# Kernel tuning notes

Measured on AMD Instinct MI355X. Metric: run time of the kernel, lower is better.

Reference implementation:

```python
import jax, jax.numpy as jnp
import numpy as np

E, NH, G = 2048, 16, 4
HD = E // NH          # head_dim = 128
KV = E // G           # kv proj width = 512 == G * HD
B, S = 2, 2048


def setup_inputs() -> dict:
    key = jax.random.key(0)
    ks = jax.random.split(key, 7)
    s = lambda n: 1.0 / np.sqrt(n)
    return {
        "query": jax.random.normal(ks[0], (B, S, E), jnp.float32),
        "key_in": jax.random.normal(ks[1], (B, S, E), jnp.float32),
        "value": jax.random.normal(ks[2], (B, S, E), jnp.float32),
        "Wq": jax.random.normal(ks[3], (E, E), jnp.float32) * s(E),
        "bq": jnp.zeros((E,), jnp.float32),
        "Wk": jax.random.normal(ks[4], (E, KV), jnp.float32) * s(E),
        "bk": jnp.zeros((KV,), jnp.float32),
        "Wv": jax.random.normal(ks[5], (E, KV), jnp.float32) * s(E),
        "bv": jnp.zeros((KV,), jnp.float32),
        "Wo": jax.random.normal(ks[6], (E, E), jnp.float32) * s(E),
        "bo": jnp.zeros((E,), jnp.float32),
    }


def reference(query, key_in, value, Wq, bq, Wk, bk, Wv, bv, Wo, bo):
    b, s, _ = query.shape
    scale = HD ** -0.5
    # projections
    q = (query @ Wq + bq).reshape(b, s, NH, HD).transpose(0, 2, 1, 3)   # [B,NH,S,HD]
    k = (key_in @ Wk + bk).reshape(b, s, G, HD).transpose(0, 2, 1, 3)   # [B,G,S,HD]
    v = (value @ Wv + bv).reshape(b, s, G, HD).transpose(0, 2, 1, 3)    # [B,G,S,HD]
    # grouped-query attention: each KV head serves NH//G query heads
    qg = q.reshape(b, G, NH // G, s, HD)                                # [B,G,NH/G,S,HD]
    scores = jnp.einsum('bgqsh,bgth->bgqst', qg, k) * scale             # [B,G,NH/G,S,S]
    w = jax.nn.softmax(scores, axis=-1)
    out = jnp.einsum('bgqst,bgth->bgqsh', w, v)                         # [B,G,NH/G,S,HD]
    out = out.reshape(b, NH, s, HD).transpose(0, 2, 1, 3).reshape(b, s, E)
    return out @ Wo + bo
```

## Files before the change

kernel.cpp:

```cpp
#include <hip/hip_runtime.h>
#include <hip/hip_bf16.h>

#define E_ 2048
#define S_ 2048
#define B_ 2
#define BS_ 4096
#define KV_ 512
#define NH_ 16
#define G_ 4
#define HD_ 128
#define QK_SCALE 0.08838834764831845f
#define LOG2E_ 1.4426950408889634f

typedef __attribute__((ext_vector_type(8))) short short8;
typedef __attribute__((ext_vector_type(4))) float floatx4;
typedef __attribute__((ext_vector_type(4))) unsigned short ushort4_;

static __device__ __forceinline__ unsigned short f2bf(float f) {
  unsigned int u = __builtin_bit_cast(unsigned int, f);
  u += 0x7fffu + ((u >> 16) & 1u);
  return (unsigned short)(u >> 16);
}

static __device__ __forceinline__ unsigned int cvt_pk_bf16(float lo, float hi) {
  unsigned int r;
  asm("v_cvt_pk_bf16_f32 %0, %1, %2" : "=v"(r) : "v"(lo), "v"(hi));
  return r;
}

static __device__ __forceinline__ void gld16(const void* g, void* l) {
  __builtin_amdgcn_global_load_lds(
      (const __attribute__((address_space(1))) unsigned int*)g,
      (__attribute__((address_space(3))) unsigned int*)l, 16, 0, 0);
}

__global__ __launch_bounds__(256) void k_prep(
    const float* __restrict__ Wq, unsigned short* __restrict__ WqT,
    const float* __restrict__ Wk, unsigned short* __restrict__ WkT,
    const float* __restrict__ Wv, unsigned short* __restrict__ WvT,
    const float* __restrict__ Wo, unsigned short* __restrict__ WoT) {
  __shared__ float ts[32][33];
  int t = blockIdx.x;
  const float* in; unsigned short* out; int N; int rem;
  if (t < 4096)      { in = Wq; out = WqT; N = 2048; rem = t; }
  else if (t < 5120) { in = Wk; out = WkT; N = 512;  rem = t - 4096; }
  else if (t < 6144) { in = Wv; out = WvT; N = 512;  rem = t - 5120; }
  else               { in = Wo; out = WoT; N = 2048; rem = t - 6144; }
  const int K = 2048;
  int nx = N >> 5;
  int bx = rem % nx, by = rem / nx;
  int tx = threadIdx.x & 31, ty = threadIdx.x >> 5;
  int n0 = bx * 32, k0 = by * 32;
#pragma unroll
  for (int i = 0; i < 4; ++i)
    ts[ty + i * 8][tx] = in[(size_t)(k0 + ty + i * 8) * N + n0 + tx];
  __syncthreads();
#pragma unroll
  for (int i = 0; i < 4; ++i)
    out[(size_t)(n0 + ty + i * 8) * K + k0 + tx] = f2bf(ts[tx][ty + i * 8]);
}

template <bool OUT_F32, bool A_F32, bool B_F32>
static __device__ __forceinline__ void gemm_bt_tile(
    const void* __restrict__ A, const void* __restrict__ Bt,
    const float* __restrict__ bias, bool rowBias, void* __restrict__ C,
    int N, int K, float scale, int bx, int by,
    unsigned short* As, unsigned short* Bs) {
  const int tid = threadIdx.x;
  const int w = tid >> 6;
  const int lhi = (tid >> 4) & 3;
  const int llo = tid & 15;
  const int wr = w >> 1, wc = w & 1;
  const size_t brow = (size_t)by * 128, bcol = (size_t)bx * 128;
  constexpr int ASTR = A_F32 ? 8192 : 4096;
  constexpr int BSTR = B_F32 ? 8192 : 4096;

  auto stage = [&](int k0, int bufi) {
    if constexpr (A_F32) {
#pragma unroll
      for (int i = 0; i < 4; ++i) {
        int o = i * 256 + tid;
        int row = o >> 3, gs = (o & 7) ^ (row & 7);
        gld16((const float*)A + (brow + row) * (size_t)K + k0 + gs * 4,
              As + bufi * ASTR + (size_t)(i * 256 + w * 64) * 8);
      }
    } else {
#pragma unroll
      for (int i = 0; i < 2; ++i) {
        int o = i * 256 + tid;
        int row = o >> 2, gs = (o & 3) ^ ((row >> 1) & 3);
        gld16((const unsigned short*)A + (brow + row) * (size_t)K + k0 + gs * 8,
              As + bufi * ASTR + (size_t)(i * 256 + w * 64) * 8);
      }
    }
    if constexpr (B_F32) {
#pragma unroll
      for (int i = 0; i < 4; ++i) {
        int o = i * 256 + tid;
        int row = o >> 3, gs = (o & 7) ^ (row & 7);
        gld16((const float*)Bt + (bcol + row) * (size_t)K + k0 + gs * 4,
              Bs + bufi * BSTR + (size_t)(i * 256 + w * 64) * 8);
      }
    } else {
#pragma unroll
      for (int i = 0; i < 2; ++i) {
        int o = i * 256 + tid;
        int row = o >> 2, gs = (o & 3) ^ ((row >> 1) & 3);
        gld16((const unsigned short*)Bt + (bcol + row) * (size_t)K + k0 + gs * 8,
              Bs + bufi * BSTR + (size_t)(i * 256 + w * 64) * 8);
      }
    }
  };

  auto frag_f32 = [&](const unsigned short* buf, int row) -> short8 {
    const char* p = (const char*)buf;
    int g0 = (lhi * 2) ^ (row & 7);
    float4 v0 = *reinterpret_cast<const float4*>(p + row * 128 + g0 * 16);
    float4 v1 = *reinterpret_cast<const float4*>(p + row * 128 + (g0 ^ 1) * 16);
    uint4 pk = {cvt_pk_bf16(v0.x, v0.y), cvt_pk_bf16(v0.z, v0.w),
                cvt_pk_bf16(v1.x, v1.y), cvt_pk_bf16(v1.z, v1.w)};
    return __builtin_bit_cast(short8, pk);
  };
  auto frag_bf = [&](const unsigned short* buf, int row) -> short8 {
    int g = lhi ^ ((row >> 1) & 3);
    return *reinterpret_cast<const short8*>((const char*)buf + row * 64 + g * 16);
  };

  floatx4 acc[4][4];
#pragma unroll
  for (int i = 0; i < 4; ++i)
#pragma unroll
    for (int j = 0; j < 4; ++j)
      acc[i][j] = (floatx4){0.f, 0.f, 0.f, 0.f};

  stage(0, 0);
  __syncthreads();
  int buf = 0;
  const int nk = K >> 5;
  for (int t = 0; t < nk; ++t) {
    if (t + 1 < nk) stage((t + 1) * 32, buf ^ 1);
    const unsigned short* Ab = As + buf * ASTR;
    const unsigned short* Bb = Bs + buf * BSTR;
    short8 a[4], b[4];
#pragma unroll
    for (int f = 0; f < 4; ++f) {
      int ra = wr * 64 + f * 16 + llo;
      int rb = wc * 64 + f * 16 + llo;
      if constexpr (A_F32)
        a[f] = frag_f32(Ab, ra);
      else
        a[f] = frag_bf(Ab, ra);
      if constexpr (B_F32)
        b[f] = frag_f32(Bb, rb);
      else
        b[f] = frag_bf(Bb, rb);
    }
    __builtin_amdgcn_s_setprio(1);
#pragma unroll
    for (int i = 0; i < 4; ++i)
#pragma unroll
      for (int j = 0; j < 4; ++j)
        acc[i][j] = __builtin_amdgcn_mfma_f32_16x16x32_bf16(a[i], b[j], acc[i][j], 0, 0, 0);
    __builtin_amdgcn_s_setprio(0);
    __syncthreads();
    buf ^= 1;
  }

  float* reg = reinterpret_cast<float*>(As) + w * 2048;
#pragma unroll
  for (int h = 0; h < 2; ++h) {
#pragma unroll
    for (int i2 = 0; i2 < 2; ++i2) {
      int i = h * 2 + i2;
#pragma unroll
      for (int j = 0; j < 4; ++j) {
#pragma unroll
        for (int r = 0; r < 4; ++r) {
          int row32 = i2 * 16 + lhi * 4 + r;
          int colx = (j * 16 + llo) ^ (lhi * 16);
          size_t grow = brow + wr * 64 + h * 32 + row32;
          size_t gc = bcol + wc * 64 + j * 16 + llo;
          float v = acc[i][j][r];
          v += rowBias ? bias[grow] : bias[gc];
          v *= scale;
          reg[row32 * 64 + colx] = v;
        }
      }
    }
#pragma unroll
    for (int p = 0; p < 8; ++p) {
      int r4 = (tid & 63) >> 4;
      int ch = tid & 15;
      int row32 = p * 4 + r4;
      int colx = (ch * 4) ^ ((p & 3) * 16);
      float4 v4 = *reinterpret_cast<const float4*>(reg + row32 * 64 + colx);
      size_t grow = brow + wr * 64 + h * 32 + row32;
      size_t gc = bcol + wc * 64 + ch * 4;
      if constexpr (OUT_F32) {
        *reinterpret_cast<float4*>((float*)C + grow * N + gc) = v4;
      } else {
        uint2 pk2;
        pk2.x = cvt_pk_bf16(v4.x, v4.y);
        pk2.y = cvt_pk_bf16(v4.z, v4.w);
        *reinterpret_cast<uint2*>((unsigned short*)C + grow * N + gc) = pk2;
      }
    }
  }
}

__global__ __launch_bounds__(256) void k_gemm_qkv(
    const float* __restrict__ query, const unsigned short* __restrict__ WqT,
    const float* __restrict__ bq, unsigned short* __restrict__ qb,
    const float* __restrict__ key_in, const unsigned short* __restrict__ WkT,
    const float* __restrict__ bk, unsigned short* __restrict__ kb,
    const unsigned short* __restrict__ WvT, const float* __restrict__ value,
    const float* __restrict__ bv, unsigned short* __restrict__ vtb) {
  __shared__ __align__(16) unsigned short lds[24576];
  int bid = blockIdx.x;
  if (bid < 512) {
    int xcd = bid & 7, u = bid >> 3;
    int by = (xcd >> 1) * 8 + (u & 7);
    int bx = (xcd & 1) * 8 + (u >> 3);
    gemm_bt_tile<false, true, false>(query, WqT, bq, false, qb, E_, E_,
                                     QK_SCALE * LOG2E_, bx, by,
                                     lds, lds + 16384);
  } else if (bid < 640) {
    int u = bid - 512;
    int cm = (u & 7) * 16 + (u >> 3);
    gemm_bt_tile<false, true, false>(key_in, WkT, bk, false, kb, KV_, E_, 1.0f,
                                     cm >> 5, cm & 31, lds, lds + 16384);
  } else {
    int u = bid - 640;
    int cm = (u & 7) * 16 + (u >> 3);
    gemm_bt_tile<false, false, true>(WvT, value, bv, true, vtb, BS_, E_, 1.0f,
                                     cm >> 2, cm & 3, lds, lds + 8192);
  }
}

__global__ __launch_bounds__(256) void k_gemm_o(
    const unsigned short* __restrict__ A, const unsigned short* __restrict__ Bt,
    const float* __restrict__ bias, float* __restrict__ C) {
  __shared__ __align__(16) unsigned short lds[16384];
  int cm = (blockIdx.x & 7) * 64 + (blockIdx.x >> 3);
  gemm_bt_tile<true, false, false>(A, Bt, bias, false, C, E_, E_, 1.0f,
                                   cm >> 5, cm & 31, lds, lds + 8192);
}

__global__ __launch_bounds__(512) void k_attn(
    const unsigned short* __restrict__ qb, const unsigned short* __restrict__ kb,
    const unsigned short* __restrict__ vt, unsigned short* __restrict__ attn) {
  __shared__ __align__(16) unsigned short Ks[2][64 * 128];
  __shared__ __align__(16) unsigned short Vs[2][128 * 64];
  __shared__ __align__(16) unsigned short Ps[8][32 * 64];

  const int tid = threadIdx.x;
  const int w = tid >> 6;
  const int lhi = (tid >> 4) & 3;
  const int llo = tid & 15;
  const int bid = blockIdx.x;
  const int xcd = bid & 7;
  const int b = xcd >> 2, g = xcd & 3;
  const int inner = bid >> 3;
  const int hq = inner & 3, qt = inner >> 2;
  const int h = g * 4 + hq;

  char* PsW = (char*)&Ps[0][0] + w * 4096;

  short8 qf[2][4];
#pragma unroll
  for (int rt = 0; rt < 2; ++rt)
#pragma unroll
    for (int hc = 0; hc < 4; ++hc) {
      int row = qt * 256 + w * 32 + rt * 16 + llo;
      qf[rt][hc] = *reinterpret_cast<const short8*>(
          qb + ((size_t)(b * 2048 + row)) * 2048 + h * 128 + hc * 32 + lhi * 8);
    }

  floatx4 acc[2][8];
#pragma unroll
  for (int rt = 0; rt < 2; ++rt)
#pragma unroll
    for (int dc = 0; dc < 8; ++dc)
      acc[rt][dc] = (floatx4){0.f, 0.f, 0.f, 0.f};
  float m_[2] = {-1e30f, -1e30f};
  float l_[2] = {0.f, 0.f};

  auto stage = [&](int kv0, int buf) {
#pragma unroll
    for (int i = 0; i < 2; ++i) {
      int o = i * 512 + tid;
      int row = o >> 4, gr2 = (o & 15) ^ (row & 7);
      gld16(kb + ((size_t)(b * 2048 + kv0 + row)) * 512 + g * 128 + gr2 * 8,
            &Ks[buf][(size_t)(i * 512 + w * 64) * 8]);
    }
#pragma unroll
    for (int i = 0; i < 2; ++i) {
      int o = i * 512 + tid;
      int row = o >> 3, gr2 = (o & 7) ^ (row & 7);
      gld16(vt + ((size_t)(g * 128 + row)) * 4096 + b * 2048 + kv0 + gr2 * 8,
            &Vs[buf][(size_t)(i * 512 + w * 64) * 8]);
    }
  };

  stage(0, 0);
  __syncthreads();
  int buf = 0;

  for (int t = 0; t < 32; ++t) {
    const int kv0 = t * 64;
    if (t < 31) stage(kv0 + 64, buf ^ 1);

    floatx4 sc[2][4];
#pragma unroll
    for (int rt = 0; rt < 2; ++rt)
#pragma unroll
      for (int c = 0; c < 4; ++c)
        sc[rt][c] = (floatx4){0.f, 0.f, 0.f, 0.f};
    __builtin_amdgcn_s_setprio(1);
#pragma unroll
    for (int c = 0; c < 4; ++c) {
      int krow = c * 16 + llo;
#pragma unroll
      for (int hc = 0; hc < 4; ++hc) {
        int byteoff = krow * 256 + ((hc * 64 + lhi * 16) ^ ((krow & 7) << 4));
        short8 kf = *reinterpret_cast<const short8*>((const char*)&Ks[buf][0] + byteoff);
        sc[0][c] = __builtin_amdgcn_mfma_f32_16x16x32_bf16(kf, qf[0][hc], sc[0][c], 0, 0, 0);
        sc[1][c] = __builtin_amdgcn_mfma_f32_16x16x32_bf16(kf, qf[1][hc], sc[1][c], 0, 0, 0);
      }
    }
    __builtin_amdgcn_s_setprio(0);

#pragma unroll
    for (int rt = 0; rt < 2; ++rt) {
      float pm = sc[rt][0][0];
#pragma unroll
      for (int c = 0; c < 4; ++c)
#pragma unroll
        for (int r = 0; r < 4; ++r) pm = fmaxf(pm, sc[rt][c][r]);
      if (__any(pm > m_[rt] + 8.0f)) {
        float t2 = pm;
        t2 = fmaxf(t2, __shfl_xor(t2, 16));
        t2 = fmaxf(t2, __shfl_xor(t2, 32));
        float m2 = fmaxf(m_[rt], t2);
        float scr = __builtin_amdgcn_exp2f(m_[rt] - m2);
        m_[rt] = m2;
        l_[rt] *= scr;
#pragma unroll
        for (int r = 0; r < 4; ++r) {
          float s_r = __shfl(scr, (tid & 48) | (((tid >> 2) & 12) + r));
#pragma unroll
          for (int dc = 0; dc < 8; ++dc) acc[rt][dc][r] *= s_r;
        }
      }
      float lsum = l_[rt];
#pragma unroll
      for (int c = 0; c < 4; ++c) {
        float e0 = __builtin_amdgcn_exp2f(sc[rt][c][0] - m_[rt]);
        float e1 = __builtin_amdgcn_exp2f(sc[rt][c][1] - m_[rt]);
        float e2 = __builtin_amdgcn_exp2f(sc[rt][c][2] - m_[rt]);
        float e3 = __builtin_amdgcn_exp2f(sc[rt][c][3] - m_[rt]);
        lsum += (e0 + e1) + (e2 + e3);
        uint2 pk;
        pk.x = cvt_pk_bf16(e0, e1);
        pk.y = cvt_pk_bf16(e2, e3);
        int byteoff = (rt * 16 + llo) * 128 + ((c * 32 + lhi * 8) ^ ((llo & 7) << 4));
        *reinterpret_cast<uint2*>(PsW + byteoff) = pk;
      }
      l_[rt] = lsum;
    }

    short8 pf[2][2];
#pragma unroll
    for (int rt = 0; rt < 2; ++rt)
#pragma unroll
      for (int kc = 0; kc < 2; ++kc) {
        int byteoff = (rt * 16 + llo) * 128 + ((kc * 64 + lhi * 16) ^ ((llo & 7) << 4));
        pf[rt][kc] = *reinterpret_cast<const short8*>(PsW + byteoff);
      }
    __builtin_amdgcn_s_setprio(1);
#pragma unroll
    for (int dc = 0; dc < 8; ++dc) {
      int vrow = dc * 16 + llo;
      int bo0 = vrow * 128 + ((lhi * 16) ^ ((vrow & 7) << 4));
      int bo1 = vrow * 128 + ((64 + lhi * 16) ^ ((vrow & 7) << 4));
      short8 vf0 = *reinterpret_cast<const short8*>((const char*)&Vs[buf][0] + bo0);
      short8 vf1 = *reinterpret_cast<const short8*>((const char*)&Vs[buf][0] + bo1);
      acc[0][dc] = __builtin_amdgcn_mfma_f32_16x16x32_bf16(pf[0][0], vf0, acc[0][dc], 0, 0, 0);
      acc[1][dc] = __builtin_amdgcn_mfma_f32_16x16x32_bf16(pf[1][0], vf0, acc[1][dc], 0, 0, 0);
      acc[0][dc] = __builtin_amdgcn_mfma_f32_16x16x32_bf16(pf[0][1], vf1, acc[0][dc], 0, 0, 0);
      acc[1][dc] = __builtin_amdgcn_mfma_f32_16x16x32_bf16(pf[1][1], vf1, acc[1][dc], 0, 0, 0);
    }
    __builtin_amdgcn_s_setprio(0);
    __syncthreads();
    buf ^= 1;
  }

#pragma unroll
  for (int rt = 0; rt < 2; ++rt) {
    float t2 = l_[rt];
    t2 += __shfl_xor(t2, 16);
    t2 += __shfl_xor(t2, 32);
    float linv = 1.0f / t2;
    float lr[4];
#pragma unroll
    for (int r = 0; r < 4; ++r)
      lr[r] = __shfl(linv, (tid & 48) | (((tid >> 2) & 12) + r));
    unsigned short* pw = (unsigned short*)PsW;
#pragma unroll
    for (int dc = 0; dc < 8; ++dc) {
      int pg = dc ^ lhi;
#pragma unroll
      for (int r = 0; r < 4; ++r)
        pw[(lhi * 4 + r) * 128 + pg * 16 + llo] = f2bf(acc[rt][dc][r] * lr[r]);
    }
    int lane = tid & 63;
#pragma unroll
    for (int p = 0; p < 4; ++p) {
      int row = p * 4 + (lane >> 4);
      int ch = lane & 15;
      uint4 v = *reinterpret_cast<const uint4*>(PsW + row * 256 + ch * 16);
      int dc = (ch >> 1) ^ (row >> 2);
      int grow = qt * 256 + w * 32 + rt * 16 + row;
      *reinterpret_cast<uint4*>(attn + ((size_t)(b * 2048 + grow)) * 2048 +
                                h * 128 + dc * 16 + (ch & 1) * 8) = v;
    }
  }
}

extern "C" void kernel_launch(void* const* d_in, const int* in_sizes, int n_in,
                              void* d_out, int out_size, void* d_ws, size_t ws_size,
                              hipStream_t stream) {
  const float* query  = (const float*)d_in[0];
  const float* key_in = (const float*)d_in[1];
  const float* value  = (const float*)d_in[2];
  const float* Wq = (const float*)d_in[3];
  const float* bq = (const float*)d_in[4];
  const float* Wk = (const float*)d_in[5];
  const float* bk = (const float*)d_in[6];
  const float* Wv = (const float*)d_in[7];
  const float* bv = (const float*)d_in[8];
  const float* Wo = (const float*)d_in[9];
  const float* bo = (const float*)d_in[10];
  float* out = (float*)d_out;

  char* ws = (char*)d_ws;
  size_t off = 0;
  auto alloc = [&](size_t bytes) {
    char* p = ws + off;
    off += (bytes + 255) & ~(size_t)255;
    return p;
  };
  unsigned short* WqT  = (unsigned short*)alloc((size_t)E_ * E_ * 2);
  unsigned short* WkT  = (unsigned short*)alloc((size_t)KV_ * E_ * 2);
  unsigned short* WvT  = (unsigned short*)alloc((size_t)KV_ * E_ * 2);
  unsigned short* WoT  = (unsigned short*)alloc((size_t)E_ * E_ * 2);
  unsigned short* qb   = (unsigned short*)alloc((size_t)BS_ * E_ * 2);
  unsigned short* kb   = (unsigned short*)alloc((size_t)BS_ * KV_ * 2);
  unsigned short* vtb  = (unsigned short*)alloc((size_t)KV_ * BS_ * 2);
  unsigned short* attb = (unsigned short*)alloc((size_t)BS_ * E_ * 2);

  k_prep<<<10240, 256, 0, stream>>>(Wq, WqT, Wk, WkT, Wv, WvT, Wo, WoT);
  k_gemm_qkv<<<768, 256, 0, stream>>>(query, WqT, bq, qb, key_in, WkT, bk, kb,
                                      WvT, value, bv, vtb);
  k_attn<<<B_ * NH_ * (S_ / 256), 512, 0, stream>>>(qb, kb, vtb, attb);
  k_gemm_o<<<512, 256, 0, stream>>>(attb, WoT, bo, out);
}
```

Baseline: 215.5 us.

## Load bf16 weight fragments directly from global memory, staging only one operand in LDS

The GEMM tile helper now stages only one operand through LDS: the fp32 activation for the QKV modes, or the bf16 A operand for the output projection. The other bf16 operand is read per-wave straight from global memory into MFMA fragments. This shrinks LDS use in the QKV kernel (from 24576 to 16384 shorts), which may allow more blocks per CU, and cuts LDS traffic. In exchange, the direct loads are uncoalesced 16-byte reads that happen every k-step without prefetch and rely on L2/L1 hits, and each wave pair reloads the same weight rows.

After: 294.8 us. 36.8% more time.

```diff
diff --git a/kernel.cpp b/kernel.cpp
--- a/kernel.cpp
+++ b/kernel.cpp
@@ -60,54 +60,40 @@
     out[(size_t)(n0 + ty + i * 8) * K + k0 + tx] = f2bf(ts[tx][ty + i * 8]);
 }
 
-template <bool OUT_F32, bool A_F32, bool B_F32>
-static __device__ __forceinline__ void gemm_bt_tile(
+template <int MODE>
+static __device__ __forceinline__ void gemm_tile(
     const void* __restrict__ A, const void* __restrict__ Bt,
     const float* __restrict__ bias, bool rowBias, void* __restrict__ C,
-    int N, int K, float scale, int bx, int by,
-    unsigned short* As, unsigned short* Bs) {
+    int N, int K, float scale, int bx, int by, unsigned short* lds) {
   const int tid = threadIdx.x;
   const int w = tid >> 6;
   const int lhi = (tid >> 4) & 3;
   const int llo = tid & 15;
   const int wr = w >> 1, wc = w & 1;
   const size_t brow = (size_t)by * 128, bcol = (size_t)bx * 128;
-  constexpr int ASTR = A_F32 ? 8192 : 4096;
-  constexpr int BSTR = B_F32 ? 8192 : 4096;
+
+  const float* fsrc = (MODE == 0) ? (const float*)A : (const float*)Bt;
+  const size_t fbase = (MODE == 0) ? brow : bcol;
+  const unsigned short* dsrc =
+      (MODE == 1) ? (const unsigned short*)A : (const unsigned short*)Bt;
+  const size_t dbase = (MODE == 1) ? (brow + wr * 64) : (bcol + wc * 64);
 
   auto stage = [&](int k0, int bufi) {
-    if constexpr (A_F32) {
-#pragma unroll
-      for (int i = 0; i < 4; ++i) {
-        int o = i * 256 + tid;
-        int row = o >> 3, gs = (o & 7) ^ (row & 7);
-        gld16((const float*)A + (brow + row) * (size_t)K + k0 + gs * 4,
-              As + bufi * ASTR + (size_t)(i * 256 + w * 64) * 8);
-      }
-    } else {
+    if constexpr (MODE == 2) {
 #pragma unroll
       for (int i = 0; i < 2; ++i) {
         int o = i * 256 + tid;
         int row = o >> 2, gs = (o & 3) ^ ((row >> 1) & 3);
         gld16((const unsigned short*)A + (brow + row) * (size_t)K + k0 + gs * 8,
-              As + bufi * ASTR + (size_t)(i * 256 + w * 64) * 8);
-      }
-    }
-    if constexpr (B_F32) {
+              lds + bufi * 4096 + (size_t)(i * 256 + w * 64) * 8);
+      }
+    } else {
 #pragma unroll
       for (int i = 0; i < 4; ++i) {
         int o = i * 256 + tid;
         int row = o >> 3, gs = (o & 7) ^ (row & 7);
-        gld16((const float*)Bt + (bcol + row) * (size_t)K + k0 + gs * 4,
-              Bs + bufi * BSTR + (size_t)(i * 256 + w * 64) * 8);
-      }
-    } else {
-#pragma unroll
-      for (int i = 0; i < 2; ++i) {
-        int o = i * 256 + tid;
-        int row = o >> 2, gs = (o & 3) ^ ((row >> 1) & 3);
-        gld16((const unsigned short*)Bt + (bcol + row) * (size_t)K + k0 + gs * 8,
-              Bs + bufi * BSTR + (size_t)(i * 256 + w * 64) * 8);
+        gld16(fsrc + (fbase + row) * (size_t)K + k0 + gs * 4,
+              lds + bufi * 8192 + (size_t)(i * 256 + w * 64) * 8);
       }
     }
   };
@@ -125,6 +111,10 @@
     int g = lhi ^ ((row >> 1) & 3);
     return *reinterpret_cast<const short8*>((const char*)buf + row * 64 + g * 16);
   };
+  auto dfrag = [&](int k0, int f) -> short8 {
+    return *reinterpret_cast<const short8*>(
+        dsrc + (dbase + f * 16 + llo) * (size_t)K + k0 + lhi * 8);
+  };
 
   floatx4 acc[4][4];
 #pragma unroll
@@ -138,35 +128,38 @@
   int buf = 0;
   const int nk = K >> 5;
   for (int t = 0; t < nk; ++t) {
-    if (t + 1 < nk) stage((t + 1) * 32, buf ^ 1);
-    const unsigned short* Ab = As + buf * ASTR;
-    const unsigned short* Bb = Bs + buf * BSTR;
-    short8 a[4], b[4];
+    const int k0 = t * 32;
+    if (t + 1 < nk) stage(k0 + 32, buf ^ 1);
+    short8 d[4];
+#pragma unroll
+    for (int f = 0; f < 4; ++f) d[f] = dfrag(k0, f);
+    short8 s[4];
 #pragma unroll
     for (int f = 0; f < 4; ++f) {
-      int ra = wr * 64 + f * 16 + llo;
-      int rb = wc * 64 + f * 16 + llo;
-      if constexpr (A_F32)
-        a[f] = frag_f32(Ab, ra);
+      if constexpr (MODE == 0)
+        s[f] = frag_f32(lds + buf * 8192, wr * 64 + f * 16 + llo);
+      else if constexpr (MODE == 1)
+        s[f] = frag_f32(lds + buf * 8192, wc * 64 + f * 16 + llo);
       else
-        a[f] = frag_bf(Ab, ra);
-      if constexpr (B_F32)
-        b[f] = frag_f32(Bb, rb);
-      else
-        b[f] = frag_bf(Bb, rb);
+        s[f] = frag_bf(lds + buf * 4096, wr * 64 + f * 16 + llo);
     }
     __builtin_amdgcn_s_setprio(1);
 #pragma unroll
     for (int i = 0; i < 4; ++i)
 #pragma unroll
-      for (int j = 0; j < 4; ++j)
-        acc[i][j] = __builtin_amdgcn_mfma_f32_16x16x32_bf16(a[i], b[j], acc[i][j], 0, 0, 0);
+      for (int j = 0; j < 4; ++j) {
+        if constexpr (MODE == 1)
+          acc[i][j] = __builtin_amdgcn_mfma_f32_16x16x32_bf16(d[i], s[j], acc[i][j], 0, 0, 0);
+        else
+          acc[i][j] = __builtin_amdgcn_mfma_f32_16x16x32_bf16(s[i], d[j], acc[i][j], 0, 0, 0);
+      }
     __builtin_amdgcn_s_setprio(0);
     __syncthreads();
     buf ^= 1;
   }
 
-  float* reg = reinterpret_cast<float*>(As) + w * 2048;
+  float* reg = reinterpret_cast<float*>(lds) + w * 2048;
+  constexpr bool OUT_F32 = (MODE == 2);
 #pragma unroll
   for (int h = 0; h < 2; ++h) {
 #pragma unroll
@@ -215,25 +208,21 @@
     const float* __restrict__ bk, unsigned short* __restrict__ kb,
     const unsigned short* __restrict__ WvT, const float* __restrict__ value,
     const float* __restrict__ bv, unsigned short* __restrict__ vtb) {
-  __shared__ __align__(16) unsigned short lds[24576];
+  __shared__ __align__(16) unsigned short lds[16384];
   int bid = blockIdx.x;
   if (bid < 512) {
     int xcd = bid & 7, u = bid >> 3;
     int by = (xcd >> 1) * 8 + (u & 7);
     int bx = (xcd & 1) * 8 + (u >> 3);
-    gemm_bt_tile<false, true, false>(query, WqT, bq, false, qb, E_, E_,
-                                     QK_SCALE * LOG2E_, bx, by,
-                                     lds, lds + 16384);
+    gemm_tile<0>(query, WqT, bq, false, qb, E_, E_, QK_SCALE * LOG2E_, bx, by, lds);
   } else if (bid < 640) {
     int u = bid - 512;
     int cm = (u & 7) * 16 + (u >> 3);
-    gemm_bt_tile<false, true, false>(key_in, WkT, bk, false, kb, KV_, E_, 1.0f,
-                                     cm >> 5, cm & 31, lds, lds + 16384);
+    gemm_tile<0>(key_in, WkT, bk, false, kb, KV_, E_, 1.0f, cm >> 5, cm & 31, lds);
   } else {
     int u = bid - 640;
     int cm = (u & 7) * 16 + (u >> 3);
-    gemm_bt_tile<false, false, true>(WvT, value, bv, true, vtb, BS_, E_, 1.0f,
-                                     cm >> 2, cm & 3, lds, lds + 8192);
+    gemm_tile<1>(WvT, value, bv, true, vtb, BS_, E_, 1.0f, cm >> 2, cm & 3, lds);
   }
 }
 
@@ -242,8 +231,7 @@
     const float* __restrict__ bias, float* __restrict__ C) {
   __shared__ __align__(16) unsigned short lds[16384];
   int cm = (blockIdx.x & 7) * 64 + (blockIdx.x >> 3);
-  gemm_bt_tile<true, false, false>(A, Bt, bias, false, C, E_, E_, 1.0f,
-                                   cm >> 5, cm & 31, lds, lds + 8192);
+  gemm_tile<2>(A, Bt, bias, false, C, E_, E_, 1.0f, cm >> 5, cm & 31, lds);
 }
 
 __global__ __launch_bounds__(512) void k_attn(
```
